# Optimization experiments

Hardware: AMD Instinct MI355X
Metric: run time of the kernel (lower is better)

Reference implementation:

```python
import jax, jax.numpy as jnp
import numpy as np

E = 768      # embed_dim (hidden_size)
H = 12       # num_attention_heads
DH = E // H  # head_dim = 64
B, S = 8, 1024


def setup_inputs() -> dict:
    key = jax.random.key(0)
    ks = jax.random.split(key, 10)
    sc = 1.0 / np.sqrt(E)
    inp = {
        "hidden_state": jax.random.normal(ks[0], (B, S, E), dtype=jnp.float32),
        # per-head Q/K/V projections, stacked over heads: [H, E, DH]
        "Wq": jax.random.normal(ks[1], (H, E, DH), dtype=jnp.float32) * sc,
        "bq": jax.random.normal(ks[2], (H, DH), dtype=jnp.float32) * 0.02,
        "Wk": jax.random.normal(ks[3], (H, E, DH), dtype=jnp.float32) * sc,
        "bk": jax.random.normal(ks[4], (H, DH), dtype=jnp.float32) * 0.02,
        "Wv": jax.random.normal(ks[5], (H, E, DH), dtype=jnp.float32) * sc,
        "bv": jax.random.normal(ks[6], (H, DH), dtype=jnp.float32) * 0.02,
        # output projection: [E, E]
        "Wo": jax.random.normal(ks[7], (E, E), dtype=jnp.float32) * sc,
        "bo": jax.random.normal(ks[8], (E,), dtype=jnp.float32) * 0.02,
    }
    return inp


def reference(hidden_state, Wq, bq, Wk, bk, Wv, bv, Wo, bo):
    # Q/K/V per head: [B,S,E] x [H,E,D] -> [B,H,S,D]
    q = jnp.einsum("bse,hed->bhsd", hidden_state, Wq) + bq[None, :, None, :]
    k = jnp.einsum("bse,hed->bhsd", hidden_state, Wk) + bk[None, :, None, :]
    v = jnp.einsum("bse,hed->bhsd", hidden_state, Wv) + bv[None, :, None, :]
    scale = 1.0 / jnp.sqrt(jnp.asarray(DH, dtype=q.dtype))
    scores = jnp.einsum("bhsd,bhtd->bhst", q, k) * scale   # [B,H,S,S]
    weights = jax.nn.softmax(scores, axis=-1)
    attn = jnp.einsum("bhst,bhtd->bhsd", weights, v)        # [B,H,S,D]
    # concat heads (head order matches ModuleList concat): [B,S,H*D]=[B,S,E]
    x = attn.transpose(0, 2, 1, 3).reshape(hidden_state.shape[0], hidden_state.shape[1], E)
    return x @ Wo + bo
```

## Files before the change

kernel.cpp:

```cpp
#include <hip/hip_runtime.h>

typedef unsigned short u16;
typedef __bf16 bf16;
typedef bf16 bf16x8 __attribute__((ext_vector_type(8)));
typedef float f32x4 __attribute__((ext_vector_type(4)));
typedef u16 u16x4 __attribute__((ext_vector_type(4)));
typedef u16 u16x8 __attribute__((ext_vector_type(8)));

#define MROWS 8192
#define EDIM 768
#define NQKV 2304
#define NHEAD 12
#define DH 64
#define SEQ 1024
#define BATCH 8
#define BH 96
#define BHSD (BH * SEQ * DH)
#define KIT64 (EDIM / 64)

#if __has_builtin(__builtin_amdgcn_exp2f)
#define EXP2(x) __builtin_amdgcn_exp2f(x)
#else
#define EXP2(x) exp2f(x)
#endif

__device__ __forceinline__ u16 f2bf(float f) {
  bf16 b = (bf16)f;
  return __builtin_bit_cast(u16, b);
}


__global__ void cvt_x(const float* __restrict__ x, u16* __restrict__ xb, int n) {
  int i = (blockIdx.x * blockDim.x + threadIdx.x) * 4;
  if (i >= n) return;
  float4 v = *(const float4*)(x + i);
  u16x4 o;
  o[0] = f2bf(v.x); o[1] = f2bf(v.y); o[2] = f2bf(v.z); o[3] = f2bf(v.w);
  *(u16x4*)(xb + i) = o;
}

__global__ __launch_bounds__(256) void pack_w(
    const float* __restrict__ Wq, const float* __restrict__ Wk,
    const float* __restrict__ Wv, const float* __restrict__ Wo,
    u16* __restrict__ Wt, u16* __restrict__ Wot) {
  __shared__ float T[64][65];
  int bid = blockIdx.x;
  int tid = threadIdx.x;
  int c = tid & 63, r4 = tid >> 6;
  if (bid < 432) {
    int region = bid / 144, rem = bid - region * 144;
    int h = rem / 12, e0 = (rem - h * 12) * 64;
    const float* W = region == 0 ? Wq : (region == 1 ? Wk : Wv);
    for (int p = 0; p < 16; p++) {
      int er = r4 + p * 4;
      T[er][c] = W[(size_t)(h * EDIM + e0 + er) * DH + c];
    }
    __syncthreads();
    int nbase = region * EDIM + h * 64;
    for (int p = 0; p < 16; p++) {
      int dr = r4 + p * 4;
      Wt[(size_t)(nbase + dr) * EDIM + e0 + c] = f2bf(T[c][dr]);
    }
  } else {
    bid -= 432;
    int n0 = (bid / 12) * 64, e0 = (bid - (bid / 12) * 12) * 64;
    for (int p = 0; p < 16; p++) {
      int er = r4 + p * 4;
      T[er][c] = Wo[(size_t)(e0 + er) * EDIM + n0 + c];
    }
    __syncthreads();
    for (int p = 0; p < 16; p++) {
      int dr = r4 + p * 4;
      Wot[(size_t)(n0 + dr) * EDIM + e0 + c] = f2bf(T[c][dr]);
    }
  }
}

__device__ __forceinline__ void gemm_core64(
    const u16* __restrict__ A, const u16* __restrict__ Bt,
    u16* As, u16* Bs,
    int m0, int n0, int tid, f32x4 acc[4][4]) {
  int wv = __builtin_amdgcn_readfirstlane(tid >> 6);
  int lane = tid & 63, quad = lane >> 4, l16 = lane & 15;
  int wm = (wv & 1) * 64, wn = (wv >> 1) * 64;
  int srow = tid >> 1;
  int cb = (tid & 1) * 4;
  const u16* Ag = A + (size_t)(m0 + srow) * EDIM + cb * 8;
  const u16* Bg = Bt + (size_t)(n0 + srow) * EDIM + cb * 8;
  int wbase = srow * 64;

  u16x8 ra[4], rb[4];
  for (int q = 0; q < 4; q++) {
    ra[q] = *(const u16x8*)(Ag + q * 8);
    rb[q] = *(const u16x8*)(Bg + q * 8);
  }
  for (int k = 0; k < KIT64; k++) {
    __syncthreads();
    for (int q = 0; q < 4; q++) {
      int sc = (((cb + q) ^ (srow & 7))) * 8;
      *(u16x8*)(As + wbase + sc) = ra[q];
      *(u16x8*)(Bs + wbase + sc) = rb[q];
    }
    __syncthreads();
    if (k + 1 < KIT64) {
      int ko = (k + 1) * 64;
      for (int q = 0; q < 4; q++) {
        ra[q] = *(const u16x8*)(Ag + ko + q * 8);
        rb[q] = *(const u16x8*)(Bg + ko + q * 8);
      }
    }
    for (int kh = 0; kh < 2; kh++) {
      bf16x8 af[4], bfr[4];
      for (int i = 0; i < 4; i++) {
        int row = wm + i * 16 + l16;
        af[i] = *(const bf16x8*)(As + row * 64 + (((kh * 4 + quad) ^ (row & 7))) * 8);
      }
      for (int j = 0; j < 4; j++) {
        int row = wn + j * 16 + l16;
        bfr[j] = *(const bf16x8*)(Bs + row * 64 + (((kh * 4 + quad) ^ (row & 7))) * 8);
      }
      for (int i = 0; i < 4; i++)
        for (int j = 0; j < 4; j++)
          acc[i][j] = __builtin_amdgcn_mfma_f32_16x16x32_bf16(af[i], bfr[j], acc[i][j], 0, 0, 0);
    }
  }
}

__global__ __launch_bounds__(256, 3) void gemm_qkv(
    const u16* __restrict__ A, const u16* __restrict__ Bt,
    const float* __restrict__ bq, const float* __restrict__ bk, const float* __restrict__ bv,
    u16* __restrict__ qkv) {
  __shared__ u16 As[128 * 64];
  __shared__ u16 Bs[128 * 64];
  int tid = threadIdx.x;
  int wv = tid >> 6, lane = tid & 63, quad = lane >> 4, l16 = lane & 15;
  int wm = (wv & 1) * 64, wn = (wv >> 1) * 64;
  int m0 = blockIdx.x * 128, n0 = blockIdx.y * 128;
  f32x4 acc[4][4] = {};
  gemm_core64(A, Bt, As, Bs, m0, n0, tid, acc);

  const float kQscale = 0.18033688011112042f;
  for (int i = 0; i < 4; i++) {
    int row0 = m0 + wm + i * 16 + quad * 4;
    for (int j = 0; j < 4; j++) {
      int n = n0 + wn + j * 16 + l16;
      int region = n / EDIM;
      int hd = n - region * EDIM;
      int h = hd >> 6, d = hd & 63;
      const float* bp = region == 0 ? bq : (region == 1 ? bk : bv);
      float bias = bp[hd];
      float scale = region == 0 ? kQscale : 1.0f;
      for (int r = 0; r < 4; r++) {
        int rr = row0 + r;
        int bb = rr >> 10, s = rr & 1023;
        float val = (acc[i][j][r] + bias) * scale;
        u16 bv16 = f2bf(val);
        int bhh = bb * NHEAD + h;
        if (region < 2) {
          qkv[(size_t)region * BHSD + ((size_t)bhh * SEQ + s) * DH + d] = bv16;
        } else {
          qkv[(size_t)2 * BHSD + ((size_t)bhh * DH + d) * SEQ + s] = bv16;
        }
      }
    }
  }
}

__global__ __launch_bounds__(256) void attn_kernel(const u16* __restrict__ qkv, u16* __restrict__ attn) {
  int bh = blockIdx.x;
  int b = bh / NHEAD, h = bh - b * NHEAD;
  const u16* Q  = qkv + (size_t)bh * SEQ * DH;
  const u16* K  = qkv + (size_t)(BH + bh) * SEQ * DH;
  const u16* VT = qkv + (size_t)(2 * BH + bh) * SEQ * DH;
  int tid = threadIdx.x, wave = tid >> 6, lane = tid & 63, quad = lane >> 4, l16 = lane & 15;
  int q_base = blockIdx.y * 128 + wave * 32;

  __shared__ u16 Ks[32 * 72];
  __shared__ u16 Vts[80 * 72];
  __shared__ u16 Ps[4][32 * 36];

  for (int i = tid; i < 16 * 64; i += 256) {
    int rr = i >> 6, cc = i & 63;
    Vts[(64 + rr) * 72 + cc] = (rr == 0) ? (u16)0x3F80 : (u16)0;
  }

  bf16x8 qf[2][2];
  for (int qi = 0; qi < 2; qi++)
    for (int c = 0; c < 2; c++)
      qf[qi][c] = *(const bf16x8*)(Q + (size_t)(q_base + qi * 16 + l16) * DH + c * 32 + quad * 8);

  f32x4 o[2][4] = {};
  f32x4 o5[2] = {};

  int tr = tid >> 3, tc8 = (tid & 7) * 8;
  int vr = tid >> 2, vc8 = (tid & 3) * 8;

  u16x8 kv = *(const u16x8*)(K + (size_t)tr * DH + tc8);
  u16x8 vv = *(const u16x8*)(VT + (size_t)vr * SEQ + vc8);

  for (int t0 = 0; t0 < SEQ; t0 += 32) {
    __syncthreads();
    *(u16x8*)(Ks + tr * 72 + tc8) = kv;
    *(u16x8*)(Vts + vr * 72 + vc8) = vv;
    __syncthreads();
    if (t0 + 32 < SEQ) {
      kv = *(const u16x8*)(K + (size_t)(t0 + 32 + tr) * DH + tc8);
      vv = *(const u16x8*)(VT + (size_t)vr * SEQ + t0 + 32 + vc8);
    }

    bf16x8 kf[2][2];
    for (int tc = 0; tc < 2; tc++)
      for (int c = 0; c < 2; c++)
        kf[tc][c] = *(const bf16x8*)(Ks + (tc * 16 + l16) * 72 + c * 32 + quad * 8);

    float p[2][2][4];
    for (int qi = 0; qi < 2; qi++)
      for (int tc = 0; tc < 2; tc++) {
        f32x4 z = {};
        z = __builtin_amdgcn_mfma_f32_16x16x32_bf16(qf[qi][0], kf[tc][0], z, 0, 0, 0);
        z = __builtin_amdgcn_mfma_f32_16x16x32_bf16(qf[qi][1], kf[tc][1], z, 0, 0, 0);
        for (int r = 0; r < 4; r++)
          p[qi][tc][r] = EXP2(z[r]);
      }

    u16* P = Ps[wave];
    for (int qi = 0; qi < 2; qi++)
      for (int tc = 0; tc < 2; tc++)
        for (int r = 0; r < 4; r++)
          P[(qi * 16 + quad * 4 + r) * 36 + tc * 16 + l16] = f2bf(p[qi][tc][r]);
    bf16x8 pf[2];
    for (int qi = 0; qi < 2; qi++)
      pf[qi] = *(const bf16x8*)(P + (qi * 16 + l16) * 36 + quad * 8);

    bf16x8 vf[4], vf5;
    for (int n = 0; n < 4; n++)
      vf[n] = *(const bf16x8*)(Vts + (n * 16 + l16) * 72 + quad * 8);
    vf5 = *(const bf16x8*)(Vts + (64 + l16) * 72 + quad * 8);

    for (int qi = 0; qi < 2; qi++) {
      for (int n = 0; n < 4; n++)
        o[qi][n] = __builtin_amdgcn_mfma_f32_16x16x32_bf16(pf[qi], vf[n], o[qi][n], 0, 0, 0);
      o5[qi] = __builtin_amdgcn_mfma_f32_16x16x32_bf16(pf[qi], vf5, o5[qi], 0, 0, 0);
    }
  }

  for (int qi = 0; qi < 2; qi++)
    for (int r = 0; r < 4; r++) {
      float s = __shfl(o5[qi][r], quad << 4);
      float inv = 1.0f / s;
      int qrow = q_base + qi * 16 + quad * 4 + r;
      size_t rowoff = (size_t)(b * SEQ + qrow) * EDIM + h * DH;
      for (int n = 0; n < 4; n++)
        attn[rowoff + n * 16 + l16] = f2bf(o[qi][n][r] * inv);
    }
}

__global__ __launch_bounds__(256, 3) void gemm_out(
    const u16* __restrict__ A, const u16* __restrict__ Bt,
    const float* __restrict__ bo, float* __restrict__ out) {
  __shared__ u16 As[128 * 64];
  __shared__ u16 Bs[128 * 64];
  int tid = threadIdx.x;
  int wv = tid >> 6, lane = tid & 63, quad = lane >> 4, l16 = lane & 15;
  int wm = (wv & 1) * 64, wn = (wv >> 1) * 64;
  int m0 = blockIdx.x * 128, n0 = blockIdx.y * 128;
  f32x4 acc[4][4] = {};
  gemm_core64(A, Bt, As, Bs, m0, n0, tid, acc);

  for (int i = 0; i < 4; i++) {
    int row0 = m0 + wm + i * 16 + quad * 4;
    for (int j = 0; j < 4; j++) {
      int n = n0 + wn + j * 16 + l16;
      float bias = bo[n];
      for (int r = 0; r < 4; r++)
        out[(size_t)(row0 + r) * EDIM + n] = acc[i][j][r] + bias;
    }
  }
}

extern "C" void kernel_launch(void* const* d_in, const int* in_sizes, int n_in,
                              void* d_out, int out_size, void* d_ws, size_t ws_size,
                              hipStream_t stream) {
  const float* x  = (const float*)d_in[0];
  const float* Wq = (const float*)d_in[1];
  const float* bq = (const float*)d_in[2];
  const float* Wk = (const float*)d_in[3];
  const float* bk = (const float*)d_in[4];
  const float* Wv = (const float*)d_in[5];
  const float* bv = (const float*)d_in[6];
  const float* Wo = (const float*)d_in[7];
  const float* bo = (const float*)d_in[8];
  float* out = (float*)d_out;
  char* ws = (char*)d_ws;

  u16* Xb   = (u16*)(ws);
  u16* Wt   = (u16*)(ws + 12582912);
  u16* Wot  = (u16*)(ws + 16121856);
  u16* qkv  = (u16*)(ws + 17301504);
  u16* attn = (u16*)(ws + 55050240);

  cvt_x<<<6144, 256, 0, stream>>>(x, Xb, MROWS * EDIM);
  pack_w<<<576, 256, 0, stream>>>(Wq, Wk, Wv, Wo, Wt, Wot);
  gemm_qkv<<<dim3(64, 18), 256, 0, stream>>>(Xb, Wt, bq, bk, bv, qkv);
  attn_kernel<<<dim3(96, 8), 256, 0, stream>>>(qkv, attn);
  gemm_out<<<dim3(64, 6), 256, 0, stream>>>(attn, Wot, bo, out);
}
```

Measured before the change: 225.3 us.

## Retile attention to 16 queries per wave and 64-key tiles

Each wave in the attention kernel now handles 16 query rows instead of 32, and each loop iteration covers 64 keys instead of 32. The grid doubles along the query dimension and launch bounds request 4 blocks per CU. The aim is more parallelism (1536 blocks), half as many barrier-separated iterations, and full-K MFMAs for the PV product. In exchange, each K/V tile loaded into shared memory is reused by half as many query rows, so total K/V traffic doubles. The P and K buffers in shared memory also grow.

```diff
diff --git a/kernel.cpp b/kernel.cpp
--- a/kernel.cpp
+++ b/kernel.cpp
@@ -166,93 +166,91 @@
   }
 }
 
-__global__ __launch_bounds__(256) void attn_kernel(const u16* __restrict__ qkv, u16* __restrict__ attn) {
+__global__ __launch_bounds__(256, 4) void attn_kernel(const u16* __restrict__ qkv, u16* __restrict__ attn) {
   int bh = blockIdx.x;
   int b = bh / NHEAD, h = bh - b * NHEAD;
   const u16* Q  = qkv + (size_t)bh * SEQ * DH;
   const u16* K  = qkv + (size_t)(BH + bh) * SEQ * DH;
   const u16* VT = qkv + (size_t)(2 * BH + bh) * SEQ * DH;
   int tid = threadIdx.x, wave = tid >> 6, lane = tid & 63, quad = lane >> 4, l16 = lane & 15;
-  int q_base = blockIdx.y * 128 + wave * 32;
-
-  __shared__ u16 Ks[32 * 72];
+  int q_base = blockIdx.y * 64 + wave * 16;
+
+  __shared__ u16 Ks[64 * 72];
   __shared__ u16 Vts[80 * 72];
-  __shared__ u16 Ps[4][32 * 36];
+  __shared__ u16 Ps[4][16 * 72];
 
   for (int i = tid; i < 16 * 64; i += 256) {
     int rr = i >> 6, cc = i & 63;
     Vts[(64 + rr) * 72 + cc] = (rr == 0) ? (u16)0x3F80 : (u16)0;
   }
 
-  bf16x8 qf[2][2];
-  for (int qi = 0; qi < 2; qi++)
-    for (int c = 0; c < 2; c++)
-      qf[qi][c] = *(const bf16x8*)(Q + (size_t)(q_base + qi * 16 + l16) * DH + c * 32 + quad * 8);
-
-  f32x4 o[2][4] = {};
-  f32x4 o5[2] = {};
+  bf16x8 qf[2];
+  for (int c = 0; c < 2; c++)
+    qf[c] = *(const bf16x8*)(Q + (size_t)(q_base + l16) * DH + c * 32 + quad * 8);
+
+  f32x4 o[4] = {};
+  f32x4 o5 = {};
 
   int tr = tid >> 3, tc8 = (tid & 7) * 8;
-  int vr = tid >> 2, vc8 = (tid & 3) * 8;
-
-  u16x8 kv = *(const u16x8*)(K + (size_t)tr * DH + tc8);
-  u16x8 vv = *(const u16x8*)(VT + (size_t)vr * SEQ + vc8);
-
-  for (int t0 = 0; t0 < SEQ; t0 += 32) {
-    __syncthreads();
-    *(u16x8*)(Ks + tr * 72 + tc8) = kv;
-    *(u16x8*)(Vts + vr * 72 + vc8) = vv;
-    __syncthreads();
-    if (t0 + 32 < SEQ) {
-      kv = *(const u16x8*)(K + (size_t)(t0 + 32 + tr) * DH + tc8);
-      vv = *(const u16x8*)(VT + (size_t)vr * SEQ + t0 + 32 + vc8);
-    }
-
-    bf16x8 kf[2][2];
-    for (int tc = 0; tc < 2; tc++)
-      for (int c = 0; c < 2; c++)
-        kf[tc][c] = *(const bf16x8*)(Ks + (tc * 16 + l16) * 72 + c * 32 + quad * 8);
-
-    float p[2][2][4];
-    for (int qi = 0; qi < 2; qi++)
-      for (int tc = 0; tc < 2; tc++) {
-        f32x4 z = {};
-        z = __builtin_amdgcn_mfma_f32_16x16x32_bf16(qf[qi][0], kf[tc][0], z, 0, 0, 0);
-        z = __builtin_amdgcn_mfma_f32_16x16x32_bf16(qf[qi][1], kf[tc][1], z, 0, 0, 0);
-        for (int r = 0; r < 4; r++)
-          p[qi][tc][r] = EXP2(z[r]);
-      }
+
+  u16x8 kv0 = *(const u16x8*)(K + (size_t)tr * DH + tc8);
+  u16x8 kv1 = *(const u16x8*)(K + (size_t)(32 + tr) * DH + tc8);
+  u16x8 vv0 = *(const u16x8*)(VT + (size_t)tr * SEQ + tc8);
+  u16x8 vv1 = *(const u16x8*)(VT + (size_t)(32 + tr) * SEQ + tc8);
+
+  for (int t0 = 0; t0 < SEQ; t0 += 64) {
+    __syncthreads();
+    *(u16x8*)(Ks + tr * 72 + tc8) = kv0;
+    *(u16x8*)(Ks + (tr + 32) * 72 + tc8) = kv1;
+    *(u16x8*)(Vts + tr * 72 + tc8) = vv0;
+    *(u16x8*)(Vts + (tr + 32) * 72 + tc8) = vv1;
+    __syncthreads();
+    if (t0 + 64 < SEQ) {
+      kv0 = *(const u16x8*)(K + (size_t)(t0 + 64 + tr) * DH + tc8);
+      kv1 = *(const u16x8*)(K + (size_t)(t0 + 96 + tr) * DH + tc8);
+      vv0 = *(const u16x8*)(VT + (size_t)tr * SEQ + t0 + 64 + tc8);
+      vv1 = *(const u16x8*)(VT + (size_t)(32 + tr) * SEQ + t0 + 64 + tc8);
+    }
+
+    float p[4][4];
+    for (int tc = 0; tc < 4; tc++) {
+      bf16x8 kf0 = *(const bf16x8*)(Ks + (tc * 16 + l16) * 72 + quad * 8);
+      bf16x8 kf1 = *(const bf16x8*)(Ks + (tc * 16 + l16) * 72 + 32 + quad * 8);
+      f32x4 z = {};
+      z = __builtin_amdgcn_mfma_f32_16x16x32_bf16(qf[0], kf0, z, 0, 0, 0);
+      z = __builtin_amdgcn_mfma_f32_16x16x32_bf16(qf[1], kf1, z, 0, 0, 0);
+      for (int r = 0; r < 4; r++)
+        p[tc][r] = EXP2(z[r]);
+    }
 
     u16* P = Ps[wave];
-    for (int qi = 0; qi < 2; qi++)
-      for (int tc = 0; tc < 2; tc++)
-        for (int r = 0; r < 4; r++)
-          P[(qi * 16 + quad * 4 + r) * 36 + tc * 16 + l16] = f2bf(p[qi][tc][r]);
+    for (int tc = 0; tc < 4; tc++)
+      for (int r = 0; r < 4; r++)
+        P[(quad * 4 + r) * 72 + tc * 16 + l16] = f2bf(p[tc][r]);
     bf16x8 pf[2];
-    for (int qi = 0; qi < 2; qi++)
-      pf[qi] = *(const bf16x8*)(P + (qi * 16 + l16) * 36 + quad * 8);
-
-    bf16x8 vf[4], vf5;
+    for (int kc = 0; kc < 2; kc++)
+      pf[kc] = *(const bf16x8*)(P + l16 * 72 + kc * 32 + quad * 8);
+
+    for (int n = 0; n < 4; n++) {
+      bf16x8 vf0 = *(const bf16x8*)(Vts + (n * 16 + l16) * 72 + quad * 8);
+      bf16x8 vf1 = *(const bf16x8*)(Vts + (n * 16 + l16) * 72 + 32 + quad * 8);
+      o[n] = __builtin_amdgcn_mfma_f32_16x16x32_bf16(pf[0], vf0, o[n], 0, 0, 0);
+      o[n] = __builtin_amdgcn_mfma_f32_16x16x32_bf16(pf[1], vf1, o[n], 0, 0, 0);
+    }
+    bf16x8 v50 = *(const bf16x8*)(Vts + (64 + l16) * 72 + quad * 8);
+    bf16x8 v51 = *(const bf16x8*)(Vts + (64 + l16) * 72 + 32 + quad * 8);
+    o5 = __builtin_amdgcn_mfma_f32_16x16x32_bf16(pf[0], v50, o5, 0, 0, 0);
+    o5 = __builtin_amdgcn_mfma_f32_16x16x32_bf16(pf[1], v51, o5, 0, 0, 0);
+  }
+
+  for (int r = 0; r < 4; r++) {
+    float s = __shfl(o5[r], quad << 4);
+    float inv = 1.0f / s;
+    int qrow = q_base + quad * 4 + r;
+    size_t rowoff = (size_t)(b * SEQ + qrow) * EDIM + h * DH;
     for (int n = 0; n < 4; n++)
-      vf[n] = *(const bf16x8*)(Vts + (n * 16 + l16) * 72 + quad * 8);
-    vf5 = *(const bf16x8*)(Vts + (64 + l16) * 72 + quad * 8);
-
-    for (int qi = 0; qi < 2; qi++) {
-      for (int n = 0; n < 4; n++)
-        o[qi][n] = __builtin_amdgcn_mfma_f32_16x16x32_bf16(pf[qi], vf[n], o[qi][n], 0, 0, 0);
-      o5[qi] = __builtin_amdgcn_mfma_f32_16x16x32_bf16(pf[qi], vf5, o5[qi], 0, 0, 0);
-    }
-  }
-
-  for (int qi = 0; qi < 2; qi++)
-    for (int r = 0; r < 4; r++) {
-      float s = __shfl(o5[qi][r], quad << 4);
-      float inv = 1.0f / s;
-      int qrow = q_base + qi * 16 + quad * 4 + r;
-      size_t rowoff = (size_t)(b * SEQ + qrow) * EDIM + h * DH;
-      for (int n = 0; n < 4; n++)
-        attn[rowoff + n * 16 + l16] = f2bf(o[qi][n][r] * inv);
-    }
+      attn[rowoff + n * 16 + l16] = f2bf(o[n][r] * inv);
+  }
 }
 
 __global__ __launch_bounds__(256, 3) void gemm_out(
@@ -302,6 +300,6 @@
   cvt_x<<<6144, 256, 0, stream>>>(x, Xb, MROWS * EDIM);
   pack_w<<<576, 256, 0, stream>>>(Wq, Wk, Wv, Wo, Wt, Wot);
   gemm_qkv<<<dim3(64, 18), 256, 0, stream>>>(Xb, Wt, bq, bk, bv, qkv);
-  attn_kernel<<<dim3(96, 8), 256, 0, stream>>>(qkv, attn);
+  attn_kernel<<<dim3(96, 16), 256, 0, stream>>>(qkv, attn);
   gemm_out<<<dim3(64, 6), 256, 0, stream>>>(attn, Wot, bo, out);
 }
```

Result: faster. 216.7 us (-3.8%).
